# Performance work log

Hardware: AMD Instinct MI355X
Metric: run time of the kernel (lower is better)

Reference implementation:

```python
import jax, jax.numpy as jnp
import numpy as np

LN_EPS = 1e-5   # torch LayerNorm default
EPS = 1e-8      # slot-attention renorm eps
ITERS = 3


def _ln(x, g, b):
    m = jnp.mean(x, axis=-1, keepdims=True)
    v = jnp.mean(jnp.square(x - m), axis=-1, keepdims=True)
    return (x - m) * jax.lax.rsqrt(v + LN_EPS) * g + b


def _gru(x, h, W_ih, W_hh, b_ih, b_hh):
    # torch GRUCell: gates ordered r, z, n; weight_* has shape [3h, in]
    gi = x @ W_ih.T + b_ih
    gh = h @ W_hh.T + b_hh
    ir, iz, inn = jnp.split(gi, 3, axis=-1)
    hr, hz, hn = jnp.split(gh, 3, axis=-1)
    r = jax.nn.sigmoid(ir + hr)
    z = jax.nn.sigmoid(iz + hz)
    n = jnp.tanh(inn + r * hn)
    return (1.0 - z) * n + z * h


def setup_inputs() -> dict:
    key = jax.random.key(0)
    ks = jax.random.split(key, 16)
    b, n, d, n_s = 32, 4096, 256, 8
    h = max(d, 128)  # hidden_dim = max(dim, hidden_dim)
    s = 1.0 / np.sqrt(d)
    inp = {
        "inputs": jax.random.normal(ks[0], (b, n, d), jnp.float32),
        "noise": jax.random.normal(ks[1], (b, n_s, d), jnp.float32),
        "slots_mu": jax.random.normal(ks[2], (1, 1, d), jnp.float32),
        "slots_logsigma": jax.random.normal(ks[3], (1, 1, d), jnp.float32) * 0.1,
        "Wq": jax.random.uniform(ks[4], (d, d), jnp.float32, -s, s),
        "bq": jnp.zeros((d,), jnp.float32),
        "Wk": jax.random.uniform(ks[5], (d, d), jnp.float32, -s, s),
        "bk": jnp.zeros((d,), jnp.float32),
        "Wv": jax.random.uniform(ks[6], (d, d), jnp.float32, -s, s),
        "bv": jnp.zeros((d,), jnp.float32),
        "W_ih": jax.random.uniform(ks[7], (3 * d, d), jnp.float32, -s, s),
        "W_hh": jax.random.uniform(ks[8], (3 * d, d), jnp.float32, -s, s),
        "b_ih": jnp.zeros((3 * d,), jnp.float32),
        "b_hh": jnp.zeros((3 * d,), jnp.float32),
        "W1": jax.random.uniform(ks[9], (h, d), jnp.float32, -s, s),
        "b1": jnp.zeros((h,), jnp.float32),
        "W2": jax.random.uniform(ks[10], (d, h), jnp.float32, -s, s),
        "b2": jnp.zeros((d,), jnp.float32),
        "g_in": jnp.ones((d,), jnp.float32), "be_in": jnp.zeros((d,), jnp.float32),
        "g_sl": jnp.ones((d,), jnp.float32), "be_sl": jnp.zeros((d,), jnp.float32),
        "g_ff": jnp.ones((d,), jnp.float32), "be_ff": jnp.zeros((d,), jnp.float32),
    }
    return inp


def reference(inputs, noise, slots_mu, slots_logsigma, Wq, bq, Wk, bk, Wv, bv,
              W_ih, W_hh, b_ih, b_hh, W1, b1, W2, b2,
              g_in, be_in, g_sl, be_sl, g_ff, be_ff):
    b, n, d = inputs.shape
    scale = d ** (-0.5)
    # reparameterized slot init
    slots = slots_mu + jnp.exp(slots_logsigma) * noise          # [b, n_s, d]
    x = _ln(inputs, g_in, be_in)
    k = x @ Wk.T + bk                                           # [b, n, d]
    v = x @ Wv.T + bv
    attn = None
    for _ in range(ITERS):
        slots_prev = slots
        q = _ln(slots, g_sl, be_sl) @ Wq.T + bq                 # [b, n_s, d]
        dots = jnp.einsum('bid,bjd->bij', q, k) * scale         # [b, n_s, n]
        attn = jax.nn.softmax(dots, axis=1)                     # softmax over SLOTS
        attn_ = attn + EPS
        attn_ = attn_ / jnp.sum(attn_, axis=-1, keepdims=True)  # renorm over inputs
        updates = jnp.einsum('bjd,bij->bid', v, attn_)          # [b, n_s, d]
        slots = _gru(updates.reshape(-1, d), slots_prev.reshape(-1, d),
                     W_ih, W_hh, b_ih, b_hh).reshape(b, -1, d)
        pre = _ln(slots, g_ff, be_ff)
        slots = slots + (jax.nn.relu(pre @ W1.T + b1) @ W2.T + b2)
    return (slots, attn)
```

## Files before the change

### kernel.cpp

```cpp
#include <hip/hip_runtime.h>
#include <hip/hip_fp16.h>
#include <cstdint>
#include <cstddef>


#define NTOK 4096
#define DDIM 256
#define NSLOT 8
#define NBATCH 32
#define NWV 64
#define SROWS (NBATCH * NSLOT)
#define NROWS (NBATCH * NTOK)
#define SCALE 0.0625f
#define LN_EPS_C 1e-5f
#define ATTN_EPS_C 1e-8f

typedef _Float16 f16x2 __attribute__((ext_vector_type(2)));
union U2H { unsigned u; f16x2 h; __half2 hh; };

__device__ __forceinline__ void wave_reduce2(float& s, float& ss) {
#pragma unroll
  for (int off = 32; off > 0; off >>= 1) {
    s  += __shfl_down(s, off, 64);
    ss += __shfl_down(ss, off, 64);
  }
}
__device__ __forceinline__ void wave_reduce2_xor(float& s, float& ss) {
#pragma unroll
  for (int off = 32; off > 0; off >>= 1) {
    s  += __shfl_xor(s, off, 64);
    ss += __shfl_xor(ss, off, 64);
  }
}

__global__ __launch_bounds__(256) void convert_weights_k(
    const float* __restrict__ Wq, const float* __restrict__ Wv,
    const float* __restrict__ Wih, const float* __restrict__ Whh,
    const float* __restrict__ W1, const float* __restrict__ W2,
    const float* __restrict__ Wk, __half* __restrict__ WqT,
    __half* __restrict__ WvT, __half* __restrict__ WihT,
    __half* __restrict__ WhhT, __half* __restrict__ W1T,
    __half* __restrict__ W2T, __half* __restrict__ Wk_h) {
  __shared__ float tile[32][33];
  int bz = blockIdx.x;
  int tx = threadIdx.x & 31, ty = threadIdx.x >> 5;
  if (bz >= 80) {
    int ro = (bz - 80) * 32, cd = blockIdx.y * 32;
#pragma unroll
    for (int p = 0; p < 32; p += 8)
      Wk_h[(size_t)(ro + ty + p) * DDIM + cd + tx] =
          __float2half(Wk[(size_t)(ro + ty + p) * DDIM + cd + tx]);
    return;
  }
  const float* in; __half* out; int O, bo;
  if (bz < 8)       { in = Wq;  out = WqT;  O = 256; bo = bz; }
  else if (bz < 16) { in = Wv;  out = WvT;  O = 256; bo = bz - 8; }
  else if (bz < 40) { in = Wih; out = WihT; O = 768; bo = bz - 16; }
  else if (bz < 64) { in = Whh; out = WhhT; O = 768; bo = bz - 40; }
  else if (bz < 72) { in = W1;  out = W1T;  O = 256; bo = bz - 64; }
  else              { in = W2;  out = W2T;  O = 256; bo = bz - 72; }
  int ro = bo * 32, cd = blockIdx.y * 32;
#pragma unroll
  for (int p = 0; p < 32; p += 8)
    tile[ty + p][tx] = in[(size_t)(ro + ty + p) * DDIM + cd + tx];
  __syncthreads();
#pragma unroll
  for (int p = 0; p < 32; p += 8)
    out[(size_t)(cd + ty + p) * O + ro + tx] = __float2half(tile[tx][ty + p]);
}

__global__ __launch_bounds__(256) void xh_prep_k(
    const float* __restrict__ X, const float* __restrict__ g,
    const float* __restrict__ be, __half* __restrict__ xh) {
  int row = blockIdx.x * 4 + (threadIdx.x >> 6);
  int lane = threadIdx.x & 63;
  float4 a = *(const float4*)(X + (size_t)row * DDIM + lane * 4);
  float s = a.x + a.y + a.z + a.w;
  float ss = a.x * a.x + a.y * a.y + a.z * a.z + a.w * a.w;
  wave_reduce2_xor(s, ss);
  float m = s * (1.f / DDIM);
  float rs = rsqrtf(ss * (1.f / DDIM) - m * m + LN_EPS_C);
  float4 gv = *(const float4*)(g + lane * 4);
  float4 bev = *(const float4*)(be + lane * 4);
  union { __half2 h[2]; uint2 u; } pk;
  pk.h[0] = __floats2half2_rn((a.x - m) * rs * gv.x + bev.x,
                              (a.y - m) * rs * gv.y + bev.y);
  pk.h[1] = __floats2half2_rn((a.z - m) * rs * gv.z + bev.z,
                              (a.w - m) * rs * gv.w + bev.w);
  *(uint2*)(xh + (size_t)row * DDIM + lane * 4) = pk.u;
}

__global__ __launch_bounds__(256) void fused_k(
    const __half* __restrict__ xh, const float* __restrict__ qk,
    const float* __restrict__ qkb, float* __restrict__ u_part,
    float* __restrict__ S_part, __half* __restrict__ ae_buf, int write_ae) {
  int b = blockIdx.x, t = threadIdx.x;
  int wv = blockIdx.y * 4 + (t >> 6);
  int lane = t & 63, half = lane >> 5, r = lane & 31;
  f16x2 qk2[NSLOT][4];
#pragma unroll
  for (int i = 0; i < NSLOT; ++i) {
    const float* qr = qk + ((size_t)b * NSLOT + i) * DDIM + r * 8;
    float4 a = *(const float4*)qr;
    float4 c = *(const float4*)(qr + 4);
    qk2[i][0] = (f16x2){(_Float16)a.x, (_Float16)a.y};
    qk2[i][1] = (f16x2){(_Float16)a.z, (_Float16)a.w};
    qk2[i][2] = (f16x2){(_Float16)c.x, (_Float16)c.y};
    qk2[i][3] = (f16x2){(_Float16)c.z, (_Float16)c.w};
  }
  float qkb_r[NSLOT];
#pragma unroll
  for (int i = 0; i < NSLOT; ++i) qkb_r[i] = qkb[b * NSLOT + i];
  float uacc[NSLOT][8] = {};
  float sacc[NSLOT] = {};
  const __half* base = xh + ((size_t)b * NTOK + (size_t)wv * 64) * DDIM;
#pragma unroll 4
  for (int p = 0; p < 32; ++p) {
    int tok = p * 2 + half;
    uint4 v = *(const uint4*)(base + (size_t)tok * DDIM + r * 8);
    U2H x0, x1, x2, x3;
    x0.u = v.x; x1.u = v.y; x2.u = v.z; x3.u = v.w;
    float dot[NSLOT];
#pragma unroll
    for (int i = 0; i < NSLOT; ++i) {
      float s = 0.f;
      s = __builtin_amdgcn_fdot2(x0.h, qk2[i][0], s, false);
      s = __builtin_amdgcn_fdot2(x1.h, qk2[i][1], s, false);
      s = __builtin_amdgcn_fdot2(x2.h, qk2[i][2], s, false);
      s = __builtin_amdgcn_fdot2(x3.h, qk2[i][3], s, false);
      dot[i] = s;
    }
#pragma unroll
    for (int i = 0; i < NSLOT; ++i) {
      dot[i] += __shfl_xor(dot[i], 1, 64);
      dot[i] += __shfl_xor(dot[i], 2, 64);
      dot[i] += __shfl_xor(dot[i], 4, 64);
      dot[i] += __shfl_xor(dot[i], 8, 64);
      dot[i] += __shfl_xor(dot[i], 16, 64);
      dot[i] += qkb_r[i];
    }
    float mx = dot[0];
#pragma unroll
    for (int i = 1; i < NSLOT; ++i) mx = fmaxf(mx, dot[i]);
    float sum = 0.f;
    float ae[NSLOT];
#pragma unroll
    for (int i = 0; i < NSLOT; ++i) { ae[i] = __expf(dot[i] - mx); sum += ae[i]; }
    float inv = 1.f / sum;
#pragma unroll
    for (int i = 0; i < NSLOT; ++i) {
      ae[i] = fmaf(ae[i], inv, ATTN_EPS_C);
      sacc[i] += ae[i];
    }
    float2 f0 = __half22float2(x0.hh);
    float2 f1 = __half22float2(x1.hh);
    float2 f2 = __half22float2(x2.hh);
    float2 f3 = __half22float2(x3.hh);
    float xf[8] = {f0.x, f0.y, f1.x, f1.y, f2.x, f2.y, f3.x, f3.y};
#pragma unroll
    for (int i = 0; i < NSLOT; ++i)
#pragma unroll
      for (int d = 0; d < 8; ++d)
        uacc[i][d] = fmaf(ae[i], xf[d], uacc[i][d]);
    if (write_ae && r == 0) {
      union { __half2 h[4]; uint4 u; } pk;
#pragma unroll
      for (int i = 0; i < 4; ++i)
        pk.h[i] = __floats2half2_rn(ae[2 * i], ae[2 * i + 1]);
      *(uint4*)(ae_buf + ((size_t)b * NTOK + wv * 64 + tok) * NSLOT) = pk.u;
    }
  }
#pragma unroll
  for (int i = 0; i < NSLOT; ++i)
#pragma unroll
    for (int d = 0; d < 8; ++d)
      uacc[i][d] += __shfl_down(uacc[i][d], 32, 64);
  if (half == 0) {
    float* up = u_part + (((size_t)b * NWV + wv) * NSLOT) * DDIM + r * 8;
#pragma unroll
    for (int i = 0; i < NSLOT; ++i) {
      float4 v0 = {uacc[i][0], uacc[i][1], uacc[i][2], uacc[i][3]};
      float4 v1 = {uacc[i][4], uacc[i][5], uacc[i][6], uacc[i][7]};
      *(float4*)(up + (size_t)i * DDIM) = v0;
      *(float4*)(up + (size_t)i * DDIM + 4) = v1;
    }
  }
#pragma unroll
  for (int i = 0; i < NSLOT; ++i) sacc[i] += __shfl_down(sacc[i], 32, 64);
  if (lane == 0) {
#pragma unroll
    for (int i = 0; i < NSLOT; ++i)
      S_part[((size_t)b * NWV + wv) * NSLOT + i] = sacc[i];
  }
}

__global__ __launch_bounds__(256) void attn_tr_k(
    const __half* __restrict__ ae_buf, float* __restrict__ attn) {
  int b = blockIdx.x;
  int tok = blockIdx.y * 256 + threadIdx.x;
  uint4 v = *(const uint4*)(ae_buf + ((size_t)b * NTOK + tok) * NSLOT);
  const __half2* h = (const __half2*)&v;
#pragma unroll
  for (int i = 0; i < 4; ++i) {
    float2 f = __half22float2(h[i]);
    attn[((size_t)b * NSLOT + 2 * i) * NTOK + tok] = f.x - ATTN_EPS_C;
    attn[((size_t)b * NSLOT + 2 * i + 1) * NTOK + tok] = f.y - ATTN_EPS_C;
  }
}

__global__ __launch_bounds__(1024) void slot_update_k(
    const float* __restrict__ u_part, const float* __restrict__ S_part,
    const float* __restrict__ slots_in, const __half* __restrict__ WvT,
    const float* __restrict__ bv, const __half* __restrict__ WihT,
    const __half* __restrict__ WhhT, const float* __restrict__ b_ih,
    const float* __restrict__ b_hh, const float* __restrict__ g_ff,
    const float* __restrict__ be_ff, const __half* __restrict__ W1T,
    const float* __restrict__ b1, const __half* __restrict__ W2T,
    const float* __restrict__ b2, const float* __restrict__ g_sl,
    const float* __restrict__ be_sl, const __half* __restrict__ WqT,
    const float* __restrict__ bq, const __half* __restrict__ Wk_h,
    const float* __restrict__ bk, const float* __restrict__ noise,
    const float* __restrict__ mu, const float* __restrict__ logsig,
    float* __restrict__ slots_out, float* __restrict__ qk,
    float* __restrict__ qkb_out, int init, int compute_qk) {
  __shared__ float red[4][6][DDIM];
  __shared__ float su[DDIM], sh[DDIM], supd[DDIM], v1[DDIM], v2[DDIM];
  __shared__ float scal[16];
  int r = blockIdx.x, t = threadIdx.x;
  int b = r >> 3, i = r & 7;
  int o = t & 255, ks = t >> 8;
  int lane = t & 63, wid = t >> 6;
  if (init) {
    if (ks == 0) {
      float ns = mu[o] + expf(logsig[o]) * noise[(size_t)r * DDIM + o];
      slots_out[(size_t)r * DDIM + o] = ns;
      v2[o] = ns;
    }
    __syncthreads();
  } else {
    {
      float up = 0.f;
      const float* upp =
          u_part + (((size_t)b * NWV + ks * 16) * NSLOT + i) * DDIM + o;
#pragma unroll
      for (int cc = 0; cc < 16; ++cc)
        up += upp[(size_t)cc * (NSLOT * DDIM)];
      red[ks][0][o] = up;
    }
    if (t < 64) {
      float sp = S_part[((size_t)b * NWV + t) * NSLOT + i];
#pragma unroll
      for (int off = 32; off > 0; off >>= 1) sp += __shfl_down(sp, off, 64);
      if (t == 0) scal[0] = sp;
    }
    if (ks == 0) sh[o] = slots_in[(size_t)r * DDIM + o];
    __syncthreads();
    if (ks == 0) {
      float invS = 1.f / scal[0];
      su[o] = (red[0][0][o] + red[1][0][o] + red[2][0][o] + red[3][0][o]) * invS;
    }
    __syncthreads();
    {
      float p = 0.f;
      const __half* wp = WvT + (size_t)(ks * 64) * DDIM + o;
#pragma unroll 8
      for (int dd = 0; dd < 64; ++dd)
        p = fmaf(su[ks * 64 + dd], __half2float(wp[(size_t)dd * DDIM]), p);
      red[ks][0][o] = p;
    }
    __syncthreads();
    if (ks == 0)
      supd[o] = bv[o] + red[0][0][o] + red[1][0][o] + red[2][0][o] + red[3][0][o];
    __syncthreads();
    {
      float p0 = 0, p1 = 0, p2 = 0, p3 = 0, p4 = 0, p5 = 0;
      const __half* pi = WihT + (size_t)(ks * 64) * (3 * DDIM) + o;
      const __half* ph = WhhT + (size_t)(ks * 64) * (3 * DDIM) + o;
#pragma unroll 4
      for (int dd = 0; dd < 64; ++dd) {
        float ud = supd[ks * 64 + dd], hd = sh[ks * 64 + dd];
        size_t off = (size_t)dd * (3 * DDIM);
        p0 = fmaf(ud, __half2float(pi[off]), p0);
        p1 = fmaf(ud, __half2float(pi[off + DDIM]), p1);
        p2 = fmaf(ud, __half2float(pi[off + 2 * DDIM]), p2);
        p3 = fmaf(hd, __half2float(ph[off]), p3);
        p4 = fmaf(hd, __half2float(ph[off + DDIM]), p4);
        p5 = fmaf(hd, __half2float(ph[off + 2 * DDIM]), p5);
      }
      red[ks][0][o] = p0; red[ks][1][o] = p1; red[ks][2][o] = p2;
      red[ks][3][o] = p3; red[ks][4][o] = p4; red[ks][5][o] = p5;
    }
    __syncthreads();
    if (ks == 0) {
      float air = b_ih[o] + red[0][0][o] + red[1][0][o] + red[2][0][o] + red[3][0][o];
      float aiz = b_ih[DDIM + o] + red[0][1][o] + red[1][1][o] + red[2][1][o] + red[3][1][o];
      float ain = b_ih[2 * DDIM + o] + red[0][2][o] + red[1][2][o] + red[2][2][o] + red[3][2][o];
      float ahr = b_hh[o] + red[0][3][o] + red[1][3][o] + red[2][3][o] + red[3][3][o];
      float ahz = b_hh[DDIM + o] + red[0][4][o] + red[1][4][o] + red[2][4][o] + red[3][4][o];
      float ahn = b_hh[2 * DDIM + o] + red[0][5][o] + red[1][5][o] + red[2][5][o] + red[3][5][o];
      float rg = 1.f / (1.f + expf(-(air + ahr)));
      float zg = 1.f / (1.f + expf(-(aiz + ahz)));
      float ng = tanhf(ain + rg * ahn);
      float nh = (1.f - zg) * ng + zg * sh[o];
      v1[o] = nh;
      float s2 = nh, ss2 = nh * nh;
      wave_reduce2(s2, ss2);
      if (lane == 0) { scal[wid] = s2; scal[4 + wid] = ss2; }
    }
    __syncthreads();
    if (ks == 0) {
      float sS = scal[0] + scal[1] + scal[2] + scal[3];
      float sQ = scal[4] + scal[5] + scal[6] + scal[7];
      float m = sS * (1.f / DDIM);
      float rs = rsqrtf(sQ * (1.f / DDIM) - m * m + LN_EPS_C);
      v2[o] = (v1[o] - m) * rs * g_ff[o] + be_ff[o];
    }
    __syncthreads();
    {
      float p = 0.f;
      const __half* wp = W1T + (size_t)(ks * 64) * DDIM + o;
#pragma unroll 8
      for (int dd = 0; dd < 64; ++dd)
        p = fmaf(v2[ks * 64 + dd], __half2float(wp[(size_t)dd * DDIM]), p);
      red[ks][0][o] = p;
    }
    __syncthreads();
    if (ks == 0)
      su[o] = fmaxf(b1[o] + red[0][0][o] + red[1][0][o] + red[2][0][o] + red[3][0][o], 0.f);
    __syncthreads();
    {
      float p = 0.f;
      const __half* wp = W2T + (size_t)(ks * 64) * DDIM + o;
#pragma unroll 8
      for (int dd = 0; dd < 64; ++dd)
        p = fmaf(su[ks * 64 + dd], __half2float(wp[(size_t)dd * DDIM]), p);
      red[ks][0][o] = p;
    }
    __syncthreads();
    if (ks == 0) {
      float out = v1[o] + b2[o] + red[0][0][o] + red[1][0][o] + red[2][0][o] + red[3][0][o];
      slots_out[(size_t)r * DDIM + o] = out;
      v2[o] = out;
    }
    __syncthreads();
  }
  if (!compute_qk) return;
  if (ks == 0) {
    float x = v2[o];
    float s2 = x, ss2 = x * x;
    wave_reduce2(s2, ss2);
    if (lane == 0) { scal[wid] = s2; scal[4 + wid] = ss2; }
  }
  __syncthreads();
  if (ks == 0) {
    float sS = scal[0] + scal[1] + scal[2] + scal[3];
    float sQ = scal[4] + scal[5] + scal[6] + scal[7];
    float m = sS * (1.f / DDIM);
    float rs = rsqrtf(sQ * (1.f / DDIM) - m * m + LN_EPS_C);
    su[o] = (v2[o] - m) * rs * g_sl[o] + be_sl[o];
  }
  __syncthreads();
  {
    float p = 0.f;
    const __half* wp = WqT + (size_t)(ks * 64) * DDIM + o;
#pragma unroll 8
    for (int dd = 0; dd < 64; ++dd)
      p = fmaf(su[ks * 64 + dd], __half2float(wp[(size_t)dd * DDIM]), p);
    red[ks][0][o] = p;
  }
  __syncthreads();
  if (ks == 0)
    sh[o] = bq[o] + red[0][0][o] + red[1][0][o] + red[2][0][o] + red[3][0][o];
  __syncthreads();
  {
    float p = 0.f;
    const __half* wp = Wk_h + (size_t)(ks * 64) * DDIM + o;
#pragma unroll 8
    for (int dd = 0; dd < 64; ++dd)
      p = fmaf(sh[ks * 64 + dd], __half2float(wp[(size_t)dd * DDIM]), p);
    red[ks][0][o] = p;
  }
  __syncthreads();
  if (ks == 0) {
    float qkv = SCALE * (red[0][0][o] + red[1][0][o] + red[2][0][o] + red[3][0][o]);
    qk[(size_t)r * DDIM + o] = qkv;
    float v0 = sh[o] * bk[o], d1 = 0.f;
    wave_reduce2(v0, d1);
    if (lane == 0) scal[wid] = v0;
  }
  __syncthreads();
  if (t == 0)
    qkb_out[r] = SCALE * (scal[0] + scal[1] + scal[2] + scal[3]);
}

extern "C" void kernel_launch(void* const* d_in, const int* in_sizes, int n_in,
                              void* d_out, int out_size, void* d_ws,
                              size_t ws_size, hipStream_t stream) {
  const float* inputs   = (const float*)d_in[0];
  const float* noise    = (const float*)d_in[1];
  const float* slots_mu = (const float*)d_in[2];
  const float* slots_ls = (const float*)d_in[3];
  const float* Wq   = (const float*)d_in[4];
  const float* bq   = (const float*)d_in[5];
  const float* Wk   = (const float*)d_in[6];
  const float* bk   = (const float*)d_in[7];
  const float* Wv   = (const float*)d_in[8];
  const float* bv   = (const float*)d_in[9];
  const float* W_ih = (const float*)d_in[10];
  const float* W_hh = (const float*)d_in[11];
  const float* b_ih = (const float*)d_in[12];
  const float* b_hh = (const float*)d_in[13];
  const float* W1   = (const float*)d_in[14];
  const float* b1   = (const float*)d_in[15];
  const float* W2   = (const float*)d_in[16];
  const float* b2   = (const float*)d_in[17];
  const float* g_in = (const float*)d_in[18];
  const float* be_in= (const float*)d_in[19];
  const float* g_sl = (const float*)d_in[20];
  const float* be_sl= (const float*)d_in[21];
  const float* g_ff = (const float*)d_in[22];
  const float* be_ff= (const float*)d_in[23];

  float* out_slots = (float*)d_out;
  float* out_attn  = (float*)d_out + SROWS * DDIM;

  float* w = (float*)d_ws;
  float* slots = w;  w += SROWS * DDIM;
  float* qk = w;     w += SROWS * DDIM;
  float* qkb = w;    w += SROWS;
  float* S_part = w; w += NBATCH * NWV * NSLOT;
  float* u_part = w; w += (size_t)NBATCH * NWV * NSLOT * DDIM;
  __half* h = (__half*)w;
  __half* xh = h;     h += (size_t)NROWS * DDIM;
  __half* ae_buf = h; h += (size_t)NROWS * NSLOT;
  __half* WqT_h = h;  h += DDIM * DDIM;
  __half* WvT_h = h;  h += DDIM * DDIM;
  __half* WihT_h = h; h += DDIM * 3 * DDIM;
  __half* WhhT_h = h; h += DDIM * 3 * DDIM;
  __half* W1T_h = h;  h += DDIM * DDIM;
  __half* W2T_h = h;  h += DDIM * DDIM;
  __half* Wk_h = h;   h += DDIM * DDIM;

  convert_weights_k<<<dim3(88, 8), 256, 0, stream>>>(
      Wq, Wv, W_ih, W_hh, W1, W2, Wk, WqT_h, WvT_h, WihT_h, WhhT_h, W1T_h,
      W2T_h, Wk_h);
  slot_update_k<<<SROWS, 1024, 0, stream>>>(
      u_part, S_part, slots, WvT_h, bv, WihT_h, WhhT_h, b_ih, b_hh, g_ff,
      be_ff, W1T_h, b1, W2T_h, b2, g_sl, be_sl, WqT_h, bq, Wk_h, bk, noise,
      slots_mu, slots_ls, slots, qk, qkb, 1, 1);
  xh_prep_k<<<NROWS / 4, 256, 0, stream>>>(inputs, g_in, be_in, xh);
  for (int it = 0; it < 3; ++it) {
    fused_k<<<dim3(NBATCH, 16), 256, 0, stream>>>(
        xh, qk, qkb, u_part, S_part, ae_buf, (it == 2) ? 1 : 0);
    float* sout = (it == 2) ? out_slots : slots;
    slot_update_k<<<SROWS, 1024, 0, stream>>>(
        u_part, S_part, slots, WvT_h, bv, WihT_h, WhhT_h, b_ih, b_hh, g_ff,
        be_ff, W1T_h, b1, W2T_h, b2, g_sl, be_sl, WqT_h, bq, Wk_h, bk, noise,
        slots_mu, slots_ls, sout, qk, qkb, 0, (it == 2) ? 0 : 1);
  }
  attn_tr_k<<<dim3(NBATCH, 16), 256, 0, stream>>>(ae_buf, out_attn);
}
```

Before: 275.2 us.

## Fuse input LayerNorm into first attention iteration and use nontemporal fp16 traffic

Replaces the standalone LayerNorm-to-fp16 prep kernel with a fused kernel that normalizes the fp32 inputs, writes the fp16 copy, and computes the first iteration's attention and partial updates in the same pass. This saves one full read of the fp16 activation buffer and one kernel launch. The fp16 store is nontemporal, and later iterations read it with nontemporal loads. The fused kernel uses fewer blocks per token (16 per batch, unroll 2), which may leave less parallelism for reading the large fp32 input.

```diff
diff --git a/kernel.cpp b/kernel.cpp
--- a/kernel.cpp
+++ b/kernel.cpp
@@ -16,6 +16,7 @@
 #define ATTN_EPS_C 1e-8f
 
 typedef _Float16 f16x2 __attribute__((ext_vector_type(2)));
+typedef unsigned int uivec4 __attribute__((ext_vector_type(4)));
 union U2H { unsigned u; f16x2 h; __half2 hh; };
 
 __device__ __forceinline__ void wave_reduce2(float& s, float& ss) {
@@ -23,13 +24,6 @@
   for (int off = 32; off > 0; off >>= 1) {
     s  += __shfl_down(s, off, 64);
     ss += __shfl_down(ss, off, 64);
-  }
-}
-__device__ __forceinline__ void wave_reduce2_xor(float& s, float& ss) {
-#pragma unroll
-  for (int off = 32; off > 0; off >>= 1) {
-    s  += __shfl_xor(s, off, 64);
-    ss += __shfl_xor(ss, off, 64);
   }
 }
 
@@ -69,25 +63,128 @@
     out[(size_t)(cd + ty + p) * O + ro + tx] = __float2half(tile[tx][ty + p]);
 }
 
-__global__ __launch_bounds__(256) void xh_prep_k(
+__global__ __launch_bounds__(256) void fused0_k(
     const float* __restrict__ X, const float* __restrict__ g,
-    const float* __restrict__ be, __half* __restrict__ xh) {
-  int row = blockIdx.x * 4 + (threadIdx.x >> 6);
-  int lane = threadIdx.x & 63;
-  float4 a = *(const float4*)(X + (size_t)row * DDIM + lane * 4);
-  float s = a.x + a.y + a.z + a.w;
-  float ss = a.x * a.x + a.y * a.y + a.z * a.z + a.w * a.w;
-  wave_reduce2_xor(s, ss);
-  float m = s * (1.f / DDIM);
-  float rs = rsqrtf(ss * (1.f / DDIM) - m * m + LN_EPS_C);
-  float4 gv = *(const float4*)(g + lane * 4);
-  float4 bev = *(const float4*)(be + lane * 4);
-  union { __half2 h[2]; uint2 u; } pk;
-  pk.h[0] = __floats2half2_rn((a.x - m) * rs * gv.x + bev.x,
-                              (a.y - m) * rs * gv.y + bev.y);
-  pk.h[1] = __floats2half2_rn((a.z - m) * rs * gv.z + bev.z,
-                              (a.w - m) * rs * gv.w + bev.w);
-  *(uint2*)(xh + (size_t)row * DDIM + lane * 4) = pk.u;
+    const float* __restrict__ be, const float* __restrict__ qk,
+    const float* __restrict__ qkb, float* __restrict__ u_part,
+    float* __restrict__ S_part, __half* __restrict__ xh) {
+  int b = blockIdx.x, t = threadIdx.x;
+  int wv = blockIdx.y * 4 + (t >> 6);
+  int lane = t & 63, half = lane >> 5, r = lane & 31;
+  f16x2 qk2[NSLOT][4];
+#pragma unroll
+  for (int i = 0; i < NSLOT; ++i) {
+    const float* qr = qk + ((size_t)b * NSLOT + i) * DDIM + r * 8;
+    float4 a = *(const float4*)qr;
+    float4 c = *(const float4*)(qr + 4);
+    qk2[i][0] = (f16x2){(_Float16)a.x, (_Float16)a.y};
+    qk2[i][1] = (f16x2){(_Float16)a.z, (_Float16)a.w};
+    qk2[i][2] = (f16x2){(_Float16)c.x, (_Float16)c.y};
+    qk2[i][3] = (f16x2){(_Float16)c.z, (_Float16)c.w};
+  }
+  float qkb_r[NSLOT];
+#pragma unroll
+  for (int i = 0; i < NSLOT; ++i) qkb_r[i] = qkb[b * NSLOT + i];
+  float4 g0 = *(const float4*)(g + r * 8);
+  float4 g1 = *(const float4*)(g + r * 8 + 4);
+  float4 be0 = *(const float4*)(be + r * 8);
+  float4 be1 = *(const float4*)(be + r * 8 + 4);
+  float uacc[NSLOT][8] = {};
+  float sacc[NSLOT] = {};
+  const float* baseX = X + ((size_t)b * NTOK + (size_t)wv * 64) * DDIM;
+  __half* baseH = xh + ((size_t)b * NTOK + (size_t)wv * 64) * DDIM;
+#pragma unroll 2
+  for (int p = 0; p < 32; ++p) {
+    int tok = p * 2 + half;
+    float4 xa = *(const float4*)(baseX + (size_t)tok * DDIM + r * 8);
+    float4 xb = *(const float4*)(baseX + (size_t)tok * DDIM + r * 8 + 4);
+    float s = xa.x + xa.y + xa.z + xa.w + xb.x + xb.y + xb.z + xb.w;
+    float ss = xa.x * xa.x + xa.y * xa.y + xa.z * xa.z + xa.w * xa.w +
+               xb.x * xb.x + xb.y * xb.y + xb.z * xb.z + xb.w * xb.w;
+#pragma unroll
+    for (int off = 1; off <= 16; off <<= 1) {
+      s += __shfl_xor(s, off, 64);
+      ss += __shfl_xor(ss, off, 64);
+    }
+    float m = s * (1.f / DDIM);
+    float rs = rsqrtf(ss * (1.f / DDIM) - m * m + LN_EPS_C);
+    float xf[8];
+    xf[0] = (xa.x - m) * rs * g0.x + be0.x;
+    xf[1] = (xa.y - m) * rs * g0.y + be0.y;
+    xf[2] = (xa.z - m) * rs * g0.z + be0.z;
+    xf[3] = (xa.w - m) * rs * g0.w + be0.w;
+    xf[4] = (xb.x - m) * rs * g1.x + be1.x;
+    xf[5] = (xb.y - m) * rs * g1.y + be1.y;
+    xf[6] = (xb.z - m) * rs * g1.z + be1.z;
+    xf[7] = (xb.w - m) * rs * g1.w + be1.w;
+    U2H h0, h1, h2, h3;
+    h0.h = (f16x2){(_Float16)xf[0], (_Float16)xf[1]};
+    h1.h = (f16x2){(_Float16)xf[2], (_Float16)xf[3]};
+    h2.h = (f16x2){(_Float16)xf[4], (_Float16)xf[5]};
+    h3.h = (f16x2){(_Float16)xf[6], (_Float16)xf[7]};
+    uivec4 pk = {h0.u, h1.u, h2.u, h3.u};
+    __builtin_nontemporal_store(
+        pk, (uivec4*)(baseH + (size_t)tok * DDIM + r * 8));
+    float dot[NSLOT];
+#pragma unroll
+    for (int i = 0; i < NSLOT; ++i) {
+      float d = 0.f;
+      d = __builtin_amdgcn_fdot2(h0.h, qk2[i][0], d, false);
+      d = __builtin_amdgcn_fdot2(h1.h, qk2[i][1], d, false);
+      d = __builtin_amdgcn_fdot2(h2.h, qk2[i][2], d, false);
+      d = __builtin_amdgcn_fdot2(h3.h, qk2[i][3], d, false);
+      dot[i] = d;
+    }
+#pragma unroll
+    for (int i = 0; i < NSLOT; ++i) {
+      dot[i] += __shfl_xor(dot[i], 1, 64);
+      dot[i] += __shfl_xor(dot[i], 2, 64);
+      dot[i] += __shfl_xor(dot[i], 4, 64);
+      dot[i] += __shfl_xor(dot[i], 8, 64);
+      dot[i] += __shfl_xor(dot[i], 16, 64);
+      dot[i] += qkb_r[i];
+    }
+    float mx = dot[0];
+#pragma unroll
+    for (int i = 1; i < NSLOT; ++i) mx = fmaxf(mx, dot[i]);
+    float sum = 0.f;
+    float ae[NSLOT];
+#pragma unroll
+    for (int i = 0; i < NSLOT; ++i) { ae[i] = __expf(dot[i] - mx); sum += ae[i]; }
+    float inv = 1.f / sum;
+#pragma unroll
+    for (int i = 0; i < NSLOT; ++i) {
+      ae[i] = fmaf(ae[i], inv, ATTN_EPS_C);
+      sacc[i] += ae[i];
+    }
+#pragma unroll
+    for (int i = 0; i < NSLOT; ++i)
+#pragma unroll
+      for (int d = 0; d < 8; ++d)
+        uacc[i][d] = fmaf(ae[i], xf[d], uacc[i][d]);
+  }
+#pragma unroll
+  for (int i = 0; i < NSLOT; ++i)
+#pragma unroll
+    for (int d = 0; d < 8; ++d)
+      uacc[i][d] += __shfl_down(uacc[i][d], 32, 64);
+  if (half == 0) {
+    float* up = u_part + (((size_t)b * NWV + wv) * NSLOT) * DDIM + r * 8;
+#pragma unroll
+    for (int i = 0; i < NSLOT; ++i) {
+      float4 v0 = {uacc[i][0], uacc[i][1], uacc[i][2], uacc[i][3]};
+      float4 v1 = {uacc[i][4], uacc[i][5], uacc[i][6], uacc[i][7]};
+      *(float4*)(up + (size_t)i * DDIM) = v0;
+      *(float4*)(up + (size_t)i * DDIM + 4) = v1;
+    }
+  }
+#pragma unroll
+  for (int i = 0; i < NSLOT; ++i) sacc[i] += __shfl_down(sacc[i], 32, 64);
+  if (lane == 0) {
+#pragma unroll
+    for (int i = 0; i < NSLOT; ++i)
+      S_part[((size_t)b * NWV + wv) * NSLOT + i] = sacc[i];
+  }
 }
 
 __global__ __launch_bounds__(256) void fused_k(
@@ -117,7 +214,8 @@
 #pragma unroll 4
   for (int p = 0; p < 32; ++p) {
     int tok = p * 2 + half;
-    uint4 v = *(const uint4*)(base + (size_t)tok * DDIM + r * 8);
+    uivec4 v = __builtin_nontemporal_load(
+        (const uivec4*)(base + (size_t)tok * DDIM + r * 8));
     U2H x0, x1, x2, x3;
     x0.u = v.x; x1.u = v.y; x2.u = v.z; x3.u = v.w;
     float dot[NSLOT];
@@ -448,8 +546,13 @@
       u_part, S_part, slots, WvT_h, bv, WihT_h, WhhT_h, b_ih, b_hh, g_ff,
       be_ff, W1T_h, b1, W2T_h, b2, g_sl, be_sl, WqT_h, bq, Wk_h, bk, noise,
       slots_mu, slots_ls, slots, qk, qkb, 1, 1);
-  xh_prep_k<<<NROWS / 4, 256, 0, stream>>>(inputs, g_in, be_in, xh);
-  for (int it = 0; it < 3; ++it) {
+  fused0_k<<<dim3(NBATCH, 16), 256, 0, stream>>>(
+      inputs, g_in, be_in, qk, qkb, u_part, S_part, xh);
+  slot_update_k<<<SROWS, 1024, 0, stream>>>(
+      u_part, S_part, slots, WvT_h, bv, WihT_h, WhhT_h, b_ih, b_hh, g_ff,
+      be_ff, W1T_h, b1, W2T_h, b2, g_sl, be_sl, WqT_h, bq, Wk_h, bk, noise,
+      slots_mu, slots_ls, slots, qk, qkb, 0, 1);
+  for (int it = 1; it < 3; ++it) {
     fused_k<<<dim3(NBATCH, 16), 256, 0, stream>>>(
         xh, qk, qkb, u_part, S_part, ae_buf, (it == 2) ? 1 : 0);
     float* sout = (it == 2) ? out_slots : slots;
```

Measured after the change: 286.4 us. 1.04x slower.
